# Optimization experiments

Hardware: AMD Instinct MI355X
Metric: run time of the kernel (lower is better)

## Reference

```python
import jax, jax.numpy as jnp
import numpy as np

EPS = 1e-8  # torch F.cosine_similarity default eps


def setup_inputs() -> dict:
    key = jax.random.key(0)
    k1, k2, k3 = jax.random.split(key, 3)
    B, S, D, O, W = 256, 10, 4096, 4096, 5
    x = jax.random.normal(k1, (B, S, D), dtype=jnp.float32)
    # Conv1d params: weight [out, in, kernel], bias [out]
    conv_w = jax.random.normal(k2, (O, D, W), dtype=jnp.float32) * (1.0 / np.sqrt(D * W))
    conv_b = jax.random.normal(k3, (O,), dtype=jnp.float32) * 0.01
    return {"x": x, "conv_w": conv_w, "conv_b": conv_b}


def reference(x, conv_w, conv_b):
    B, S, D = x.shape
    # central frame: original code uses index S//2 + 1 (faithful off-by-one)
    central = x[:, S // 2 + 1, :]  # [B, D]
    dots = jnp.einsum('bsd,bd->bs', x, central)  # [B, S]
    xn = jnp.maximum(jnp.linalg.norm(x, axis=-1), EPS)      # [B, S]
    cn = jnp.maximum(jnp.linalg.norm(central, axis=-1), EPS)  # [B]
    cos = dots / (xn * cn[:, None])  # [B, S]
    # original multiplies by RAW (unnormalized) cosine weights
    xw = x * cos[:, :, None]  # [B, S, D]
    # conv1d over time: [B, D, S] -> [B, O, S-W+1]
    y = jax.lax.conv_general_dilated(
        jnp.transpose(xw, (0, 2, 1)), conv_w,
        window_strides=(1,), padding='VALID',
        dimension_numbers=('NCH', 'OIH', 'NCH'))
    y = y + conv_b[None, :, None]
    return jnp.mean(y, axis=-1)  # [B, O]
```

## Files before the change

kernel.cpp:

```cpp
#include <hip/hip_runtime.h>


#define BDIM 256
#define SEQ 10
#define DDIM 4096
#define ODIM 4096
#define WDIM 5
#define GK 20480
#define SPLITS 8
#define KSPLIT (GK / SPLITS)
#define KITERS (KSPLIT / 32)

typedef __bf16 bf16x8 __attribute__((ext_vector_type(8)));
typedef float f32x4 __attribute__((ext_vector_type(4)));

__device__ __forceinline__ unsigned short f2bf(float f) {
    union { float f; unsigned v; } c; c.f = f;
    unsigned r = c.v + 0x7FFFu + ((c.v >> 16) & 1u);
    return (unsigned short)(r >> 16);
}
__device__ __forceinline__ void async16(void* lds, const void* g) {
    __builtin_amdgcn_global_load_lds(
        (const __attribute__((address_space(1))) void*)g,
        (__attribute__((address_space(3))) void*)lds, 16, 0, 0);
}

__global__ __launch_bounds__(256) void cos_kernel(const float* __restrict__ x,
                                                  float* __restrict__ cosv)
{
    const int b = blockIdx.x;
    const int tid = threadIdx.x;
    const float* xb = x + (size_t)b * SEQ * DDIM;
    float dot[SEQ], sq[SEQ];
#pragma unroll
    for (int s = 0; s < SEQ; ++s) { dot[s] = 0.f; sq[s] = 0.f; }

    for (int base = 0; base < DDIM; base += 1024) {
        const int d = base + tid * 4;
        const f32x4 c4 = *(const f32x4*)(xb + 6 * DDIM + d);
#pragma unroll
        for (int s = 0; s < SEQ; ++s) {
            const f32x4 v4 = *(const f32x4*)(xb + s * DDIM + d);
            dot[s] += v4[0] * c4[0] + v4[1] * c4[1] + v4[2] * c4[2] + v4[3] * c4[3];
            sq[s]  += v4[0] * v4[0] + v4[1] * v4[1] + v4[2] * v4[2] + v4[3] * v4[3];
        }
    }
#pragma unroll
    for (int s = 0; s < SEQ; ++s) {
#pragma unroll
        for (int off = 32; off > 0; off >>= 1) {
            dot[s] += __shfl_down(dot[s], off, 64);
            sq[s]  += __shfl_down(sq[s], off, 64);
        }
    }
    __shared__ float red[4][2 * SEQ];
    const int wave = tid >> 6, lane = tid & 63;
    if (lane == 0) {
#pragma unroll
        for (int s = 0; s < SEQ; ++s) { red[wave][s] = dot[s]; red[wave][SEQ + s] = sq[s]; }
    }
    __syncthreads();
    if (tid == 0) {
        const float S6 = red[0][SEQ + 6] + red[1][SEQ + 6] + red[2][SEQ + 6] + red[3][SEQ + 6];
        const float cn = fmaxf(sqrtf(S6), 1e-8f);
#pragma unroll
        for (int s = 0; s < SEQ; ++s) {
            const float Dv = red[0][s] + red[1][s] + red[2][s] + red[3][s];
            const float Sv = red[0][SEQ + s] + red[1][SEQ + s] + red[2][SEQ + s] + red[3][SEQ + s];
            cosv[b * SEQ + s] = Dv / (fmaxf(sqrtf(Sv), 1e-8f) * cn);
        }
    }
}

__global__ __launch_bounds__(256) void build_p_kernel(const float* __restrict__ x,
                                                      const float* __restrict__ cosv,
                                                      unsigned short* __restrict__ P)
{
    const int b = blockIdx.x >> 2;
    const int chunk = blockIdx.x & 3;
    const int d0 = chunk * 1024 + threadIdx.x * 4;
    __shared__ float cs[SEQ];
    if (threadIdx.x < SEQ) cs[threadIdx.x] = cosv[b * SEQ + threadIdx.x];
    __syncthreads();

    const float* xb = x + (size_t)b * SEQ * DDIM + d0;
    float sc[SEQ][4];
#pragma unroll
    for (int s = 0; s < SEQ; ++s) {
        const f32x4 v4 = *(const f32x4*)(xb + s * DDIM);
        const float c = cs[s];
        sc[s][0] = v4[0] * c; sc[s][1] = v4[1] * c;
        sc[s][2] = v4[2] * c; sc[s][3] = v4[3] * c;
    }
    __attribute__((aligned(16))) unsigned short o[20];
#pragma unroll
    for (int w = 0; w < WDIM; ++w) {
#pragma unroll
        for (int j = 0; j < 4; ++j) {
            const float p = sc[w][j] + sc[w + 1][j] + sc[w + 2][j] +
                            sc[w + 3][j] + sc[w + 4][j] + sc[w + 5][j];
            o[j * WDIM + w] = f2bf(p);
        }
    }
    unsigned short* dst = P + ((size_t)b * DDIM + d0) * WDIM;
#pragma unroll
    for (int q = 0; q < 5; ++q)
        *(uint2*)(dst + q * 4) = *(const uint2*)(o + q * 4);
}

__global__ __launch_bounds__(256) void gemm_splitk_kernel(const unsigned short* __restrict__ A,
                                                          const float* __restrict__ W,
                                                          float* __restrict__ Cpart)
{
    const int bid = blockIdx.x;
    const int nt = bid & 63;
    const int sp = bid >> 6;
    const int tid = threadIdx.x;
    const int lane = tid & 63;
    const int wave = tid >> 6;

    __shared__ __align__(16) unsigned short lds_a[256 * 32];
    __shared__ __align__(16) unsigned short lds_w[64 * 32];

    f32x4 acc[4][4];
#pragma unroll
    for (int i = 0; i < 4; ++i)
#pragma unroll
        for (int j = 0; j < 4; ++j)
            acc[i][j] = (f32x4){0.f, 0.f, 0.f, 0.f};

    int k0 = sp * KSPLIT;

    const int arow_lo = tid >> 2;
    const int apq = tid & 3;

    const int wrow = tid >> 2;
    const int wcq = tid & 3;
    const float* wsrc = W + ((size_t)(nt * 64 + wrow)) * GK + wcq * 8;
    unsigned short* wdst = lds_w + wrow * 32 + ((wcq ^ (wrow & 3)) * 8);

    const int fm = lane & 15;
    const int fg = lane >> 4;
    const unsigned short* ard[4];
    const unsigned short* wrd[4];
#pragma unroll
    for (int i = 0; i < 4; ++i) {
        const int ra = wave * 64 + i * 16 + fm;
        ard[i] = lds_a + ra * 32 + ((fg ^ (ra & 3)) * 8);
        const int rw = i * 16 + fm;
        wrd[i] = lds_w + rw * 32 + ((fg ^ (rw & 3)) * 8);
    }

    for (int it = 0; it < KITERS; ++it) {
#pragma unroll
        for (int q = 0; q < 4; ++q) {
            const int row = q * 64 + arow_lo;
            const char* src = (const char*)(A + (size_t)row * GK + k0) + ((apq ^ (row & 3)) * 16);
            async16((char*)lds_a + q * 4096 + tid * 16, src);
        }
        {
            const f32x4 w0 = *(const f32x4*)(wsrc + k0);
            const f32x4 w1 = *(const f32x4*)(wsrc + k0 + 4);
            bf16x8 wb;
#pragma unroll
            for (int e = 0; e < 4; ++e) { wb[e] = (__bf16)w0[e]; wb[4 + e] = (__bf16)w1[e]; }
            *(bf16x8*)wdst = wb;
        }
        __syncthreads();

        bf16x8 af[4], wf[4];
#pragma unroll
        for (int i = 0; i < 4; ++i) af[i] = *(const bf16x8*)ard[i];
#pragma unroll
        for (int j = 0; j < 4; ++j) wf[j] = *(const bf16x8*)wrd[j];
#pragma unroll
        for (int i = 0; i < 4; ++i)
#pragma unroll
            for (int j = 0; j < 4; ++j)
                acc[i][j] = __builtin_amdgcn_mfma_f32_16x16x32_bf16(af[i], wf[j], acc[i][j], 0, 0, 0);
        __syncthreads();
        k0 += 32;
    }

    float* Cp = Cpart + (size_t)sp * (BDIM * ODIM);
    const int mbase = wave * 64 + fg * 4;
    const int nbase = nt * 64 + fm;
#pragma unroll
    for (int i = 0; i < 4; ++i)
#pragma unroll
        for (int j = 0; j < 4; ++j) {
            const int n = nbase + j * 16;
#pragma unroll
            for (int r = 0; r < 4; ++r) {
                const int m = mbase + i * 16 + r;
                Cp[(size_t)m * ODIM + n] = acc[i][j][r];
            }
        }
}

__global__ __launch_bounds__(256) void reduce_kernel(const float* __restrict__ part,
                                                     const float* __restrict__ bias,
                                                     float* __restrict__ out)
{
    const int idx = (blockIdx.x * 256 + threadIdx.x) * 4;
    f32x4 s = (f32x4){0.f, 0.f, 0.f, 0.f};
#pragma unroll
    for (int sp = 0; sp < SPLITS; ++sp) {
        const f32x4 v = *(const f32x4*)(part + (size_t)sp * (BDIM * ODIM) + idx);
        s[0] += v[0]; s[1] += v[1]; s[2] += v[2]; s[3] += v[3];
    }
    const int n = idx & (ODIM - 1);
    const f32x4 b4 = *(const f32x4*)(bias + n);
    const float inv6 = 1.0f / 6.0f;
    f32x4 o;
#pragma unroll
    for (int e = 0; e < 4; ++e) o[e] = s[e] * inv6 + b4[e];
    *(f32x4*)(out + idx) = o;
}

extern "C" void kernel_launch(void* const* d_in, const int* in_sizes, int n_in,
                              void* d_out, int out_size, void* d_ws, size_t ws_size,
                              hipStream_t stream) {
    const float* x  = (const float*)d_in[0];
    const float* cw = (const float*)d_in[1];
    const float* cb = (const float*)d_in[2];
    float* out = (float*)d_out;

    char* ws = (char*)d_ws;
    float* cosv = (float*)ws;
    unsigned short* P = (unsigned short*)(ws + 16384);
    float* parts = (float*)(ws + 16384 + (size_t)BDIM * GK * 2);

    hipLaunchKernelGGL(cos_kernel,         dim3(256),  dim3(256), 0, stream, x, cosv);
    hipLaunchKernelGGL(build_p_kernel,     dim3(1024), dim3(256), 0, stream, x, cosv, P);
    hipLaunchKernelGGL(gemm_splitk_kernel, dim3(512),  dim3(256), 0, stream, P, cw, parts);
    hipLaunchKernelGGL(reduce_kernel,      dim3(1024), dim3(256), 0, stream, parts, cb, out);
}
```

Baseline: 519.0 us.

## Double-buffer GEMM K-loop with BK=64 and fuse cosine and P-build kernels

The split-K GEMM now uses two LDS buffers and a K tile of 64. The next tile's A async loads and W global loads are issued before computing the current tile, which hides global memory latency behind MFMA work and halves the number of barriers. The block index mapping is changed so the 8 split-K blocks of the same N tile are adjacent, and launch bounds request 2 blocks per CU. The cosine kernel is fused with the P-construction kernel, removing one launch and the cosv round trip; the trade-off is that only 256 blocks now do that work and x is re-read within one block.

```diff
diff --git a/kernel.cpp b/kernel.cpp
--- a/kernel.cpp
+++ b/kernel.cpp
@@ -9,7 +9,8 @@
 #define GK 20480
 #define SPLITS 8
 #define KSPLIT (GK / SPLITS)
-#define KITERS (KSPLIT / 32)
+#define BK 64
+#define KITERS (KSPLIT / BK)
 
 typedef __bf16 bf16x8 __attribute__((ext_vector_type(8)));
 typedef float f32x4 __attribute__((ext_vector_type(4)));
@@ -25,12 +26,13 @@
         (__attribute__((address_space(3))) void*)lds, 16, 0, 0);
 }
 
-__global__ __launch_bounds__(256) void cos_kernel(const float* __restrict__ x,
-                                                  float* __restrict__ cosv)
+__global__ __launch_bounds__(256) void cosp_kernel(const float* __restrict__ x,
+                                                   unsigned short* __restrict__ P)
 {
     const int b = blockIdx.x;
     const int tid = threadIdx.x;
     const float* xb = x + (size_t)b * SEQ * DDIM;
+
     float dot[SEQ], sq[SEQ];
 #pragma unroll
     for (int s = 0; s < SEQ; ++s) { dot[s] = 0.f; sq[s] = 0.f; }
@@ -54,6 +56,7 @@
         }
     }
     __shared__ float red[4][2 * SEQ];
+    __shared__ float cs[SEQ];
     const int wave = tid >> 6, lane = tid & 63;
     if (lane == 0) {
 #pragma unroll
@@ -67,60 +70,55 @@
         for (int s = 0; s < SEQ; ++s) {
             const float Dv = red[0][s] + red[1][s] + red[2][s] + red[3][s];
             const float Sv = red[0][SEQ + s] + red[1][SEQ + s] + red[2][SEQ + s] + red[3][SEQ + s];
-            cosv[b * SEQ + s] = Dv / (fmaxf(sqrtf(Sv), 1e-8f) * cn);
-        }
-    }
-}
-
-__global__ __launch_bounds__(256) void build_p_kernel(const float* __restrict__ x,
-                                                      const float* __restrict__ cosv,
-                                                      unsigned short* __restrict__ P)
-{
-    const int b = blockIdx.x >> 2;
-    const int chunk = blockIdx.x & 3;
-    const int d0 = chunk * 1024 + threadIdx.x * 4;
-    __shared__ float cs[SEQ];
-    if (threadIdx.x < SEQ) cs[threadIdx.x] = cosv[b * SEQ + threadIdx.x];
+            cs[s] = Dv / (fmaxf(sqrtf(Sv), 1e-8f) * cn);
+        }
+    }
     __syncthreads();
 
-    const float* xb = x + (size_t)b * SEQ * DDIM + d0;
-    float sc[SEQ][4];
-#pragma unroll
-    for (int s = 0; s < SEQ; ++s) {
-        const f32x4 v4 = *(const f32x4*)(xb + s * DDIM);
-        const float c = cs[s];
-        sc[s][0] = v4[0] * c; sc[s][1] = v4[1] * c;
-        sc[s][2] = v4[2] * c; sc[s][3] = v4[3] * c;
-    }
-    __attribute__((aligned(16))) unsigned short o[20];
-#pragma unroll
-    for (int w = 0; w < WDIM; ++w) {
-#pragma unroll
-        for (int j = 0; j < 4; ++j) {
-            const float p = sc[w][j] + sc[w + 1][j] + sc[w + 2][j] +
-                            sc[w + 3][j] + sc[w + 4][j] + sc[w + 5][j];
-            o[j * WDIM + w] = f2bf(p);
-        }
-    }
-    unsigned short* dst = P + ((size_t)b * DDIM + d0) * WDIM;
-#pragma unroll
-    for (int q = 0; q < 5; ++q)
-        *(uint2*)(dst + q * 4) = *(const uint2*)(o + q * 4);
-}
-
-__global__ __launch_bounds__(256) void gemm_splitk_kernel(const unsigned short* __restrict__ A,
-                                                          const float* __restrict__ W,
-                                                          float* __restrict__ Cpart)
+    float csr[SEQ];
+#pragma unroll
+    for (int s = 0; s < SEQ; ++s) csr[s] = cs[s];
+
+    for (int chunk = 3; chunk >= 0; --chunk) {
+        const int d0 = chunk * 1024 + tid * 4;
+        const float* xd = xb + d0;
+        float sc[SEQ][4];
+#pragma unroll
+        for (int s = 0; s < SEQ; ++s) {
+            const f32x4 v4 = *(const f32x4*)(xd + s * DDIM);
+            sc[s][0] = v4[0] * csr[s]; sc[s][1] = v4[1] * csr[s];
+            sc[s][2] = v4[2] * csr[s]; sc[s][3] = v4[3] * csr[s];
+        }
+        __attribute__((aligned(16))) unsigned short o[20];
+#pragma unroll
+        for (int w = 0; w < WDIM; ++w) {
+#pragma unroll
+            for (int j = 0; j < 4; ++j) {
+                const float p = sc[w][j] + sc[w + 1][j] + sc[w + 2][j] +
+                                sc[w + 3][j] + sc[w + 4][j] + sc[w + 5][j];
+                o[j * WDIM + w] = f2bf(p);
+            }
+        }
+        unsigned short* dst = P + ((size_t)b * DDIM + d0) * WDIM;
+#pragma unroll
+        for (int q = 0; q < 5; ++q)
+            *(uint2*)(dst + q * 4) = *(const uint2*)(o + q * 4);
+    }
+}
+
+__global__ __launch_bounds__(256, 2) void gemm_splitk_kernel(const unsigned short* __restrict__ A,
+                                                             const float* __restrict__ W,
+                                                             float* __restrict__ Cpart)
 {
     const int bid = blockIdx.x;
-    const int nt = bid & 63;
-    const int sp = bid >> 6;
+    const int sp = bid & 7;
+    const int nt = bid >> 3;
     const int tid = threadIdx.x;
     const int lane = tid & 63;
     const int wave = tid >> 6;
 
-    __shared__ __align__(16) unsigned short lds_a[256 * 32];
-    __shared__ __align__(16) unsigned short lds_w[64 * 32];
+    __shared__ __align__(16) unsigned short lds_a[2][256 * BK];
+    __shared__ __align__(16) unsigned short lds_w[2][64 * BK];
 
     f32x4 acc[4][4];
 #pragma unroll
@@ -129,58 +127,89 @@
         for (int j = 0; j < 4; ++j)
             acc[i][j] = (f32x4){0.f, 0.f, 0.f, 0.f};
 
-    int k0 = sp * KSPLIT;
-
-    const int arow_lo = tid >> 2;
-    const int apq = tid & 3;
-
-    const int wrow = tid >> 2;
-    const int wcq = tid & 3;
-    const float* wsrc = W + ((size_t)(nt * 64 + wrow)) * GK + wcq * 8;
-    unsigned short* wdst = lds_w + wrow * 32 + ((wcq ^ (wrow & 3)) * 8);
+    const int s_arow = tid >> 3;
+    const int s_aoct = tid & 7;
+
+    const int s_wrow = tid >> 2;
+    const float* wsrc = W + ((size_t)(nt * 64 + s_wrow)) * GK + (tid & 3) * 16;
+    const int wo0 = (((tid & 3) * 2)     ^ (s_wrow & 7)) * 8;
+    const int wo1 = (((tid & 3) * 2 + 1) ^ (s_wrow & 7)) * 8;
 
     const int fm = lane & 15;
     const int fg = lane >> 4;
-    const unsigned short* ard[4];
-    const unsigned short* wrd[4];
+    int aoff[2][4], woff[2][4];
 #pragma unroll
     for (int i = 0; i < 4; ++i) {
         const int ra = wave * 64 + i * 16 + fm;
-        ard[i] = lds_a + ra * 32 + ((fg ^ (ra & 3)) * 8);
         const int rw = i * 16 + fm;
-        wrd[i] = lds_w + rw * 32 + ((fg ^ (rw & 3)) * 8);
-    }
-
-    for (int it = 0; it < KITERS; ++it) {
-#pragma unroll
-        for (int q = 0; q < 4; ++q) {
-            const int row = q * 64 + arow_lo;
-            const char* src = (const char*)(A + (size_t)row * GK + k0) + ((apq ^ (row & 3)) * 16);
-            async16((char*)lds_a + q * 4096 + tid * 16, src);
-        }
-        {
-            const f32x4 w0 = *(const f32x4*)(wsrc + k0);
-            const f32x4 w1 = *(const f32x4*)(wsrc + k0 + 4);
-            bf16x8 wb;
-#pragma unroll
-            for (int e = 0; e < 4; ++e) { wb[e] = (__bf16)w0[e]; wb[4 + e] = (__bf16)w1[e]; }
-            *(bf16x8*)wdst = wb;
-        }
+#pragma unroll
+        for (int kh = 0; kh < 2; ++kh) {
+            aoff[kh][i] = ra * BK + (((kh * 4 + fg) ^ (ra & 7)) * 8);
+            woff[kh][i] = rw * BK + (((kh * 4 + fg) ^ (rw & 7)) * 8);
+        }
+    }
+
+#define STAGE_A(buf, kk)                                                        \
+    _Pragma("unroll")                                                           \
+    for (int q = 0; q < 8; ++q) {                                               \
+        const int row_ = q * 32 + s_arow;                                       \
+        const unsigned short* src_ =                                            \
+            A + (size_t)row_ * GK + (kk) + ((s_aoct ^ (row_ & 7)) * 8);         \
+        async16((char*)&lds_a[buf][0] + q * 4096 + tid * 16, src_);             \
+    }
+
+#define LOAD_W(kk)                                                              \
+    w0 = *(const f32x4*)(wsrc + (kk));                                          \
+    w1 = *(const f32x4*)(wsrc + (kk) + 4);                                      \
+    w2 = *(const f32x4*)(wsrc + (kk) + 8);                                      \
+    w3 = *(const f32x4*)(wsrc + (kk) + 12);
+
+#define WRITE_W(buf)                                                            \
+    {                                                                           \
+        bf16x8 lo_, hi_;                                                        \
+        _Pragma("unroll")                                                       \
+        for (int e = 0; e < 4; ++e) {                                           \
+            lo_[e] = (__bf16)w0[e]; lo_[4 + e] = (__bf16)w1[e];                 \
+            hi_[e] = (__bf16)w2[e]; hi_[4 + e] = (__bf16)w3[e];                 \
+        }                                                                       \
+        *(bf16x8*)&lds_w[buf][s_wrow * BK + wo0] = lo_;                         \
+        *(bf16x8*)&lds_w[buf][s_wrow * BK + wo1] = hi_;                         \
+    }
+
+#define COMPUTE(buf)                                                            \
+    _Pragma("unroll")                                                           \
+    for (int kh = 0; kh < 2; ++kh) {                                            \
+        bf16x8 af[4], wf[4];                                                    \
+        _Pragma("unroll")                                                       \
+        for (int i = 0; i < 4; ++i) af[i] = *(const bf16x8*)&lds_a[buf][aoff[kh][i]]; \
+        _Pragma("unroll")                                                       \
+        for (int j = 0; j < 4; ++j) wf[j] = *(const bf16x8*)&lds_w[buf][woff[kh][j]]; \
+        _Pragma("unroll")                                                       \
+        for (int i = 0; i < 4; ++i)                                             \
+            _Pragma("unroll")                                                   \
+            for (int j = 0; j < 4; ++j)                                         \
+                acc[i][j] = __builtin_amdgcn_mfma_f32_16x16x32_bf16(            \
+                    af[i], wf[j], acc[i][j], 0, 0, 0);                          \
+    }
+
+    int k0 = sp * KSPLIT;
+    f32x4 w0, w1, w2, w3;
+
+    STAGE_A(0, k0);
+    LOAD_W(k0);
+    WRITE_W(0);
+    __syncthreads();
+
+    for (int it = 0; it < KITERS - 1; ++it) {
+        const int cur = it & 1, nxt = cur ^ 1;
+        STAGE_A(nxt, k0 + BK);
+        LOAD_W(k0 + BK);
+        COMPUTE(cur);
+        WRITE_W(nxt);
         __syncthreads();
-
-        bf16x8 af[4], wf[4];
-#pragma unroll
-        for (int i = 0; i < 4; ++i) af[i] = *(const bf16x8*)ard[i];
-#pragma unroll
-        for (int j = 0; j < 4; ++j) wf[j] = *(const bf16x8*)wrd[j];
-#pragma unroll
-        for (int i = 0; i < 4; ++i)
-#pragma unroll
-            for (int j = 0; j < 4; ++j)
-                acc[i][j] = __builtin_amdgcn_mfma_f32_16x16x32_bf16(af[i], wf[j], acc[i][j], 0, 0, 0);
-        __syncthreads();
-        k0 += 32;
-    }
+        k0 += BK;
+    }
+    COMPUTE((KITERS - 1) & 1);
 
     float* Cp = Cpart + (size_t)sp * (BDIM * ODIM);
     const int mbase = wave * 64 + fg * 4;
@@ -196,6 +225,10 @@
                 Cp[(size_t)m * ODIM + n] = acc[i][j][r];
             }
         }
+#undef STAGE_A
+#undef LOAD_W
+#undef WRITE_W
+#undef COMPUTE
 }
 
 __global__ __launch_bounds__(256) void reduce_kernel(const float* __restrict__ part,
@@ -227,12 +260,10 @@
     float* out = (float*)d_out;
 
     char* ws = (char*)d_ws;
-    float* cosv = (float*)ws;
     unsigned short* P = (unsigned short*)(ws + 16384);
     float* parts = (float*)(ws + 16384 + (size_t)BDIM * GK * 2);
 
-    hipLaunchKernelGGL(cos_kernel,         dim3(256),  dim3(256), 0, stream, x, cosv);
-    hipLaunchKernelGGL(build_p_kernel,     dim3(1024), dim3(256), 0, stream, x, cosv, P);
+    hipLaunchKernelGGL(cosp_kernel,        dim3(256),  dim3(256), 0, stream, x, P);
     hipLaunchKernelGGL(gemm_splitk_kernel, dim3(512),  dim3(256), 0, stream, P, cw, parts);
     hipLaunchKernelGGL(reduce_kernel,      dim3(1024), dim3(256), 0, stream, parts, cb, out);
 }
```

After: 501.3 us. 1.04x faster.
